# Optimization experiments

Hardware: AMD Instinct MI355X
Metric: run time of the kernel (lower is better)

The kernel has to match this reference:

```python
import jax, jax.numpy as jnp
import numpy as np

EMBED = 768
NH = 12          # num_heads
NL = 3           # num_levels
NP = 4           # num_points
DV = 384         # value dim = embed_dim * deform_ratio(0.5)
DH = DV // NH    # per-head value dim = 32
B = 16
LQ = 1024        # (512/16)^2 ViT tokens
SHAPES = [(64, 64), (32, 32), (16, 16)]  # 1/8, 1/16, 1/32 pyramid of 512x512
LKV = sum(h * w for h, w in SHAPES)      # 5376
EPS = 1e-6


def layer_norm(x, w, b):
    mu = jnp.mean(x, axis=-1, keepdims=True)
    var = jnp.mean((x - mu) ** 2, axis=-1, keepdims=True)
    return (x - mu) / jnp.sqrt(var + EPS) * w + b


def bilinear_sample(v, loc, H, W):
    # v: (B, NH, H*W, DH); loc: (B, Lq, NH, P, 2) normalized in [0,1]
    # Matches torch grid_sample(align_corners=False, padding_mode='zeros').
    Bv, Lq = loc.shape[0], loc.shape[1]
    x = loc[..., 0] * W - 0.5
    y = loc[..., 1] * H - 0.5
    x0 = jnp.floor(x)
    y0 = jnp.floor(y)
    dx = x - x0
    dy = y - y0
    x0i = x0.astype(jnp.int32)
    y0i = y0.astype(jnp.int32)

    def gather(xi, yi):
        valid = (xi >= 0) & (xi < W) & (yi >= 0) & (yi < H)  # (B,Lq,NH,P)
        xc = jnp.clip(xi, 0, W - 1)
        yc = jnp.clip(yi, 0, H - 1)
        lin = (yc * W + xc).transpose(0, 2, 1, 3).reshape(Bv, NH, Lq * NP)
        g = jnp.take_along_axis(v, lin[..., None], axis=2)  # (B,NH,Lq*P,DH)
        g = g.reshape(Bv, NH, Lq, NP, DH).transpose(0, 2, 1, 3, 4)  # (B,Lq,NH,P,DH)
        return g * valid[..., None].astype(g.dtype)

    g00 = gather(x0i, y0i)
    g01 = gather(x0i + 1, y0i)
    g10 = gather(x0i, y0i + 1)
    g11 = gather(x0i + 1, y0i + 1)
    w00 = ((1 - dx) * (1 - dy))[..., None]
    w01 = (dx * (1 - dy))[..., None]
    w10 = ((1 - dx) * dy)[..., None]
    w11 = (dx * dy)[..., None]
    return g00 * w00 + g01 * w01 + g10 * w10 + g11 * w11


def ms_deform_attn_core(value, shapes_list, loc, aw):
    # value: (B,LKV,NH,DH); loc: (B,Lq,NH,NL,NP,2); aw: (B,Lq,NH,NL,NP)
    Bv, Lq = loc.shape[0], loc.shape[1]
    samples = []
    idx = 0
    for l, (H, W) in enumerate(shapes_list):
        v = value[:, idx:idx + H * W].transpose(0, 2, 1, 3)  # (B,NH,HW,DH)
        idx += H * W
        samples.append(bilinear_sample(v, loc[:, :, :, l], H, W))
    s = jnp.stack(samples, axis=3)  # (B,Lq,NH,NL,NP,DH)
    o = jnp.einsum('bqhlp,bqhlpd->bqhd', aw, s)
    return o.reshape(Bv, Lq, NH * DH)


def setup_inputs() -> dict:
    key = jax.random.key(0)
    ks = jax.random.split(key, 12)

    def n(k, shape, s=0.02):
        return jax.random.normal(k, shape, jnp.float32) * s

    return {
        'q': jax.random.normal(ks[0], (B, LQ, EMBED), jnp.float32),
        'reference_points': jax.random.uniform(ks[1], (B, LQ, NL, 2), jnp.float32),
        'kv': jax.random.normal(ks[2], (B, LKV, EMBED), jnp.float32),
        'spatial_shapes': jnp.asarray(SHAPES, jnp.int32),
        'level_start_index': jnp.asarray(
            np.cumsum([0] + [h * w for h, w in SHAPES])[:-1], jnp.int32),
        'ln1_w': jnp.ones(EMBED, jnp.float32),
        'ln1_b': jnp.zeros(EMBED, jnp.float32),
        'ln2_w': jnp.ones(EMBED, jnp.float32),
        'ln2_b': jnp.zeros(EMBED, jnp.float32),
        'gamma': n(ks[3], (EMBED,), 0.1),
        'w_off': n(ks[4], (EMBED, NH * NL * NP * 2)),
        'b_off': n(ks[5], (NH * NL * NP * 2,), 0.01),
        'w_aw': n(ks[6], (EMBED, NH * NL * NP)),
        'b_aw': jnp.zeros(NH * NL * NP, jnp.float32),
        'w_val': n(ks[7], (EMBED, DV)),
        'b_val': jnp.zeros(DV, jnp.float32),
        'w_out': n(ks[8], (DV, EMBED)),
        'b_out': jnp.zeros(EMBED, jnp.float32),
    }


def reference(q, reference_points, kv, spatial_shapes, level_start_index,
              ln1_w, ln1_b, ln2_w, ln2_b, gamma,
              w_off, b_off, w_aw, b_aw, w_val, b_val, w_out, b_out):
    shapes_list = [tuple(int(v) for v in r) for r in np.asarray(spatial_shapes)]
    Bq, Lq, _ = q.shape
    qn = layer_norm(q, ln1_w, ln1_b)
    kvn = layer_norm(kv, ln2_w, ln2_b)
    value = (kvn @ w_val + b_val).reshape(Bq, -1, NH, DH)
    off = (qn @ w_off + b_off).reshape(Bq, Lq, NH, NL, NP, 2)
    aw = (qn @ w_aw + b_aw).reshape(Bq, Lq, NH, NL * NP)
    aw = jax.nn.softmax(aw, axis=-1).reshape(Bq, Lq, NH, NL, NP)
    # offset normalizer is (W_l, H_l) per level
    wh = jnp.asarray([[w, h] for (h, w) in shapes_list], q.dtype)  # (NL,2)
    loc = reference_points[:, :, None, :, None, :] + off / wh[None, None, None, :, None, :]
    attn = ms_deform_attn_core(value, shapes_list, loc, aw)
    attn = attn @ w_out + b_out
    return q + gamma * attn
```

## Files before the change

### kernel.cpp

```cpp
#include <hip/hip_runtime.h>

#define DEV __device__ __forceinline__

typedef short bf16x8 __attribute__((ext_vector_type(8)));
typedef short short8 __attribute__((ext_vector_type(8)));
typedef float f32x4 __attribute__((ext_vector_type(4)));
typedef unsigned int u32;
typedef __attribute__((address_space(1))) const u32* gas_ptr;
typedef __attribute__((address_space(3))) u32* las_ptr;

DEV short f2bf(float f) {
  union { float f; unsigned u; } un; un.f = f;
  unsigned r = un.u + 0x7FFFu + ((un.u >> 16) & 1u);
  return (short)(r >> 16);
}
DEV float bf2f(unsigned short s) {
  union { unsigned u; float f; } un;
  un.u = ((unsigned)s) << 16;
  return un.f;
}
DEV void gload16(const short* g, short* l) {
  __builtin_amdgcn_global_load_lds((gas_ptr)g, (las_ptr)l, 16, 0, 0);
}
DEV float hsum4(float4 v) { return v.x + v.y + v.z + v.w; }

DEV void ln_row4(const float* __restrict__ x, const float* __restrict__ w,
                 const float* __restrict__ b, short* __restrict__ y,
                 const int rb) {
  const int wv = threadIdx.x >> 6, lane = threadIdx.x & 63;
  const int row = rb * 4 + wv;
  const float* xr = x + (size_t)row * 768;
  float4 v0 = *(const float4*)(xr + lane * 4);
  float4 v1 = *(const float4*)(xr + 256 + lane * 4);
  float4 v2 = *(const float4*)(xr + 512 + lane * 4);
  float s = hsum4(v0) + hsum4(v1) + hsum4(v2);
  #pragma unroll
  for (int off = 32; off > 0; off >>= 1) s += __shfl_xor(s, off, 64);
  const float mu = s * (1.f / 768.f);
  float4 d0 = make_float4(v0.x - mu, v0.y - mu, v0.z - mu, v0.w - mu);
  float4 d1 = make_float4(v1.x - mu, v1.y - mu, v1.z - mu, v1.w - mu);
  float4 d2 = make_float4(v2.x - mu, v2.y - mu, v2.z - mu, v2.w - mu);
  float vs = d0.x * d0.x + d0.y * d0.y + d0.z * d0.z + d0.w * d0.w +
             d1.x * d1.x + d1.y * d1.y + d1.z * d1.z + d1.w * d1.w +
             d2.x * d2.x + d2.y * d2.y + d2.z * d2.z + d2.w * d2.w;
  #pragma unroll
  for (int off = 32; off > 0; off >>= 1) vs += __shfl_xor(vs, off, 64);
  const float rs = rsqrtf(vs * (1.f / 768.f) + 1e-6f);
  const float4 w0 = *(const float4*)(w + lane * 4);
  const float4 w1 = *(const float4*)(w + 256 + lane * 4);
  const float4 w2 = *(const float4*)(w + 512 + lane * 4);
  const float4 b0 = *(const float4*)(b + lane * 4);
  const float4 b1 = *(const float4*)(b + 256 + lane * 4);
  const float4 b2 = *(const float4*)(b + 512 + lane * 4);
  unsigned short* yr = (unsigned short*)y + (size_t)row * 768;
  ushort4 o;
  o.x = (unsigned short)f2bf(d0.x * rs * w0.x + b0.x);
  o.y = (unsigned short)f2bf(d0.y * rs * w0.y + b0.y);
  o.z = (unsigned short)f2bf(d0.z * rs * w0.z + b0.z);
  o.w = (unsigned short)f2bf(d0.w * rs * w0.w + b0.w);
  *(ushort4*)(yr + lane * 4) = o;
  o.x = (unsigned short)f2bf(d1.x * rs * w1.x + b1.x);
  o.y = (unsigned short)f2bf(d1.y * rs * w1.y + b1.y);
  o.z = (unsigned short)f2bf(d1.z * rs * w1.z + b1.z);
  o.w = (unsigned short)f2bf(d1.w * rs * w1.w + b1.w);
  *(ushort4*)(yr + 256 + lane * 4) = o;
  o.x = (unsigned short)f2bf(d2.x * rs * w2.x + b2.x);
  o.y = (unsigned short)f2bf(d2.y * rs * w2.y + b2.y);
  o.z = (unsigned short)f2bf(d2.z * rs * w2.z + b2.z);
  o.w = (unsigned short)f2bf(d2.w * rs * w2.w + b2.w);
  *(ushort4*)(yr + 512 + lane * 4) = o;
}

__global__ __launch_bounds__(256) void fused_pre_kernel(
    const float* __restrict__ kv, const float* __restrict__ q,
    const float* __restrict__ ln2w, const float* __restrict__ ln2b,
    const float* __restrict__ ln1w, const float* __restrict__ ln1b,
    short* __restrict__ kvn, short* __restrict__ qn,
    const float* __restrict__ w_val, const float* __restrict__ w_off,
    const float* __restrict__ w_aw, const float* __restrict__ w_out,
    const float* __restrict__ b_off, const float* __restrict__ b_aw,
    short* __restrict__ wT_val, short* __restrict__ wT_offaw,
    short* __restrict__ wT_out, float* __restrict__ bias_cat) {
  const int bid = blockIdx.x;
  if (bid < 21504) { ln_row4(kv, ln2w, ln2b, kvn, bid); return; }
  if (bid < 25600) { ln_row4(q, ln1w, ln1b, qn, bid - 21504); return; }
  int g = (bid - 25600) * 256 + threadIdx.x;
  bf16x8 v;
  if (g < 36864) {
    int n = g / 96, k0 = (g % 96) * 8;
    #pragma unroll
    for (int i = 0; i < 8; i++) v[i] = f2bf(w_val[(size_t)(k0 + i) * 384 + n]);
    *(bf16x8*)&wT_val[n * 768 + k0] = v;
    return;
  }
  g -= 36864;
  if (g < 27648) {
    int n = g / 96, k0 = (g % 96) * 8;
    #pragma unroll
    for (int i = 0; i < 8; i++) v[i] = f2bf(w_off[(size_t)(k0 + i) * 288 + n]);
    *(bf16x8*)&wT_offaw[n * 768 + k0] = v;
    return;
  }
  g -= 27648;
  if (g < 13824) {
    int n = g / 96, k0 = (g % 96) * 8;
    #pragma unroll
    for (int i = 0; i < 8; i++) v[i] = f2bf(w_aw[(size_t)(k0 + i) * 144 + n]);
    *(bf16x8*)&wT_offaw[(288 + n) * 768 + k0] = v;
    return;
  }
  g -= 13824;
  if (g < 7680) {
    int n = 432 + g / 96, k0 = (g % 96) * 8;
    #pragma unroll
    for (int i = 0; i < 8; i++) v[i] = 0;
    *(bf16x8*)&wT_offaw[n * 768 + k0] = v;
    return;
  }
  g -= 7680;
  if (g < 36864) {
    int n = g / 48, k0 = (g % 48) * 8;
    #pragma unroll
    for (int i = 0; i < 8; i++) v[i] = f2bf(w_out[(size_t)(k0 + i) * 768 + n]);
    *(bf16x8*)&wT_out[n * 384 + k0] = v;
    return;
  }
  g -= 36864;
  if (g < 512) { bias_cat[g] = (g < 288) ? b_off[g] : (g < 432 ? b_aw[g - 288] : 0.f); }
}

DEV void gemm_core(const short* __restrict__ A, const short* __restrict__ Wt,
                   const int K, const int row0, const int n0,
                   short* As, short* Bs, f32x4 acc[4][4]) {
  const int tid = threadIdx.x;
  const int wave = tid >> 6, lane = tid & 63;
  const int lr = lane & 15, quad = lane >> 4;
  const int wm = wave >> 1, wn = wave & 1;

  const short* gA[2]; const short* gB[2];
  int loA[2];
  #pragma unroll
  for (int rnd = 0; rnd < 2; rnd++) {
    int G = rnd * 256 + wave * 64 + lane;
    int line = G >> 3, pos = G & 7, x = pos ^ (line & 7);
    int r = line * 2 + (x >> 2), qk = (x & 3) * 8;
    gA[rnd] = A + (size_t)(row0 + r) * K + qk;
    gB[rnd] = Wt + (size_t)(n0 + r) * K + qk;
    loA[rnd] = (rnd * 256 + wave * 64) * 8;
  }

  int aOff[4], bOff[4];
  #pragma unroll
  for (int t4 = 0; t4 < 4; t4++) {
    int r = wm * 64 + t4 * 16 + lr;
    int pos = ((r & 1) * 4 + quad) ^ ((r >> 1) & 7);
    aOff[t4] = ((r >> 1) * 8 + pos) * 8;
    int rb = wn * 64 + t4 * 16 + lr;
    int posb = ((rb & 1) * 4 + quad) ^ ((rb >> 1) & 7);
    bOff[t4] = ((rb >> 1) * 8 + posb) * 8;
  }

  #pragma unroll
  for (int i = 0; i < 4; i++)
    #pragma unroll
    for (int j = 0; j < 4; j++)
      #pragma unroll
      for (int e = 0; e < 4; e++) acc[i][j][e] = 0.f;

  const int nt = K >> 5;
  #pragma unroll
  for (int pb = 0; pb < 2; pb++) {
    const int bb = pb * 4096;
    gload16(gA[0], As + bb + loA[0]);
    gload16(gA[1], As + bb + loA[1]);
    gload16(gB[0], Bs + bb + loA[0]);
    gload16(gB[1], Bs + bb + loA[1]);
    gA[0] += 32; gA[1] += 32; gB[0] += 32; gB[1] += 32;
  }

  int cur = 0;
  for (int t = 0; t < nt; ++t) {
    if (t + 2 < nt) {
      const int nb = (cur == 0 ? 2 : cur - 1) * 4096;
      gload16(gA[0], As + nb + loA[0]);
      gload16(gA[1], As + nb + loA[1]);
      gload16(gB[0], Bs + nb + loA[0]);
      gload16(gB[1], Bs + nb + loA[1]);
      gA[0] += 32; gA[1] += 32; gB[0] += 32; gB[1] += 32;
      asm volatile("s_waitcnt vmcnt(8)" ::: "memory");
    } else if (t + 1 < nt) {
      asm volatile("s_waitcnt vmcnt(4)" ::: "memory");
    } else {
      asm volatile("s_waitcnt vmcnt(0)" ::: "memory");
    }
    asm volatile("s_barrier" ::: "memory");
    const int cb = cur * 4096;
    bf16x8 av[4], bv[4];
    #pragma unroll
    for (int t4 = 0; t4 < 4; t4++) {
      av[t4] = *(const bf16x8*)(As + cb + aOff[t4]);
      bv[t4] = *(const bf16x8*)(Bs + cb + bOff[t4]);
    }
    #pragma unroll
    for (int ct = 0; ct < 4; ct++)
      #pragma unroll
      for (int rt = 0; rt < 4; rt++)
        acc[rt][ct] = __builtin_amdgcn_mfma_f32_16x16x32_bf16(av[rt], bv[ct], acc[rt][ct], 0, 0, 0);
    asm volatile("s_waitcnt lgkmcnt(0)" ::: "memory");
    __builtin_amdgcn_sched_barrier(0);
    asm volatile("s_barrier" ::: "memory");
    cur = (cur == 2) ? 0 : cur + 1;
  }
}

template <bool RES>
DEV void epilogue_f32(float* lds, f32x4 acc[4][4], const float* __restrict__ bias,
                      const float* __restrict__ qres, const float* __restrict__ gamma,
                      float* __restrict__ Cout, const int N,
                      const int row0, const int n0) {
  const int tid = threadIdx.x, wave = tid >> 6, lane = tid & 63;
  const int lr = lane & 15, quad = lane >> 4;
  const int wm = wave >> 1, wn = wave & 1;
  const int ST = 132;
  #pragma unroll
  for (int ph = 0; ph < 2; ++ph) {
    __syncthreads();
    if (wm == ph) {
      #pragma unroll
      for (int ct = 0; ct < 4; ct++)
        #pragma unroll
        for (int rt = 0; rt < 4; rt++)
          #pragma unroll
          for (int i = 0; i < 4; i++)
            lds[(rt * 16 + quad * 4 + i) * ST + wn * 64 + ct * 16 + lr] = acc[rt][ct][i];
    }
    __syncthreads();
    #pragma unroll
    for (int it = 0; it < 8; ++it) {
      const int slot = it * 256 + tid;
      const int r = slot >> 5, c4 = slot & 31;
      const float4 v = *(float4*)&lds[r * ST + c4 * 4];
      const int m = row0 + ph * 64 + r, n = n0 + c4 * 4;
      const float4 bs = *(const float4*)&bias[n];
      float4 o;
      if (RES) {
        const float4 qv = *(const float4*)&qres[(size_t)m * N + n];
        const float4 gm = *(const float4*)&gamma[n];
        o.x = qv.x + gm.x * (v.x + bs.x);
        o.y = qv.y + gm.y * (v.y + bs.y);
        o.z = qv.z + gm.z * (v.z + bs.z);
        o.w = qv.w + gm.w * (v.w + bs.w);
      } else {
        o.x = v.x + bs.x; o.y = v.y + bs.y; o.z = v.z + bs.z; o.w = v.w + bs.w;
      }
      *(float4*)&Cout[(size_t)m * N + n] = o;
    }
  }
}

DEV void epilogue_bf16(unsigned short* lds, f32x4 acc[4][4],
                       const float* __restrict__ bias,
                       unsigned short* __restrict__ Cout, const int N,
                       const int row0, const int n0) {
  const int tid = threadIdx.x, wave = tid >> 6, lane = tid & 63;
  const int lr = lane & 15, quad = lane >> 4;
  const int wm = wave >> 1, wn = wave & 1;
  const int ST = 136;
  #pragma unroll
  for (int ph = 0; ph < 2; ++ph) {
    __syncthreads();
    if (wm == ph) {
      #pragma unroll
      for (int ct = 0; ct < 4; ct++) {
        const float bs = bias[n0 + wn * 64 + ct * 16 + lr];
        #pragma unroll
        for (int rt = 0; rt < 4; rt++)
          #pragma unroll
          for (int i = 0; i < 4; i++)
            lds[(rt * 16 + quad * 4 + i) * ST + wn * 64 + ct * 16 + lr] =
                (unsigned short)f2bf(acc[rt][ct][i] + bs);
      }
    }
    __syncthreads();
    #pragma unroll
    for (int it = 0; it < 4; ++it) {
      const int slot = it * 256 + tid;
      const int r = slot >> 4, c8 = slot & 15;
      const short8 v = *(short8*)&lds[r * ST + c8 * 8];
      const int m = row0 + ph * 64 + r;
      *(short8*)&Cout[(size_t)m * N + n0 + c8 * 8] = v;
    }
  }
}

__global__ __launch_bounds__(256, 3) void gemm_dual_kernel(
    const short* __restrict__ A0, const short* __restrict__ W0,
    const float* __restrict__ b0, short* __restrict__ C0,
    const short* __restrict__ A1, const short* __restrict__ W1,
    const float* __restrict__ b1, float* __restrict__ C1) {
  __shared__ __align__(16) char smem[49152];
  short* As = (short*)smem;
  short* Bs = (short*)(smem + 24576);
  const int id = blockIdx.x;
  const int swz = (id & 7) * 316 + (id >> 3);
  const bool isval = swz < 2016;
  const short* A; const short* Wt; const float* bias;
  int row0, n0;
  if (isval) {
    A = A0; Wt = W0; bias = b0;
    n0 = (swz % 3) * 128; row0 = (swz / 3) * 128;
  } else {
    const int o = swz - 2016;
    A = A1; Wt = W1; bias = b1;
    n0 = (o & 3) * 128; row0 = (o >> 2) * 128;
  }
  f32x4 acc[4][4];
  gemm_core(A, Wt, 768, row0, n0, As, Bs, acc);
  if (isval) {
    epilogue_bf16((unsigned short*)smem, acc, bias, (unsigned short*)C0, 384, row0, n0);
  } else {
    epilogue_f32<false>((float*)smem, acc, bias, nullptr, nullptr, C1, 512, row0, n0);
  }
}

__global__ __launch_bounds__(256, 3) void gemm_final_kernel(
    const short* __restrict__ A, const short* __restrict__ Wt,
    const float* __restrict__ bias, const float* __restrict__ qres,
    const float* __restrict__ gamma, float* __restrict__ Cout) {
  __shared__ __align__(16) char smem[49152];
  short* As = (short*)smem;
  short* Bs = (short*)(smem + 24576);
  const int id = blockIdx.x;
  const int swz = (id & 7) * 96 + (id >> 3);
  const int n0 = (swz % 6) * 128, row0 = (swz / 6) * 128;
  f32x4 acc[4][4];
  gemm_core(A, Wt, 384, row0, n0, As, Bs, acc);
  epilogue_f32<true>((float*)smem, acc, bias, qres, gamma, Cout, 768, row0, n0);
}

__global__ __launch_bounds__(384) void sampler_kernel(
    const float* __restrict__ offaw,
    const float* __restrict__ refp,
    const short* __restrict__ value,
    short* __restrict__ o) {
  const int tid = threadIdx.x;
  const int blk = (blockIdx.x & 7) * 512 + (blockIdx.x >> 3);
  const int bq0 = blk * 4;
  __shared__ __align__(16) float s[4][440];
  __shared__ float sref[4][6];
  __shared__ float snw[48][12];
  __shared__ __align__(8) ushort4 slin[576];
  __shared__ __align__(16) float4 sw[576];

  {
    const int qi = tid / 96, t = tid % 96;
    const float* row = offaw + (size_t)(bq0 + qi) * 512;
    #pragma unroll
    for (int i = t; i < 108; i += 96)
      *(float4*)&s[qi][i * 4] = *(const float4*)&row[i * 4];
    if (t < 6) sref[qi][t] = refp[(size_t)(bq0 + qi) * 6 + t];
  }
  __syncthreads();

  if (tid < 48) {
    const int qi = tid / 12, h = tid % 12;
    const float* awp = &s[qi][288 + h * 12];
    float mx = awp[0];
    #pragma unroll
    for (int j = 1; j < 12; j++) mx = fmaxf(mx, awp[j]);
    float e[12], ssum = 0.f;
    #pragma unroll
    for (int j = 0; j < 12; j++) { e[j] = __expf(awp[j] - mx); ssum += e[j]; }
    const float inv = 1.f / ssum;
    #pragma unroll
    for (int j = 0; j < 12; j++) snw[tid][j] = e[j] * inv;
  }
  for (int tu = tid; tu < 576; tu += 384) {
    const int qi = tu / 144, rem = tu % 144;
    const int h = rem / 12, lp = rem % 12, l = lp >> 2, p = lp & 3;
    const int Wi = 64 >> l;
    const float Wf = (float)Wi;
    const float rx = sref[qi][l * 2], ry = sref[qi][l * 2 + 1];
    const int oi = ((h * 3 + l) * 4 + p) * 2;
    float x = fmaf(rx, Wf, s[qi][oi] - 0.5f);
    float y = fmaf(ry, Wf, s[qi][oi + 1] - 0.5f);
    float xf = floorf(x), yf = floorf(y);
    float dx = x - xf, dy = y - yf;
    int x0 = (int)xf, y0 = (int)yf;
    int x1 = x0 + 1, y1 = y0 + 1;
    int x0c = min(max(x0, 0), Wi - 1), x1c = min(max(x1, 0), Wi - 1);
    int y0c = min(max(y0, 0), Wi - 1), y1c = min(max(y1, 0), Wi - 1);
    float wx0 = (x0 >= 0 && x0 < Wi) ? (1.f - dx) : 0.f;
    float wx1 = (x1 < Wi && x1 >= 0) ? dx : 0.f;
    float wy0 = (y0 >= 0 && y0 < Wi) ? (1.f - dy) : 0.f;
    float wy1 = (y1 < Wi && y1 >= 0) ? dy : 0.f;
    const int st = (l == 0) ? 0 : (l == 1 ? 4096 : 5120);
    ushort4 lv;
    lv.x = (unsigned short)(st + y0c * Wi + x0c);
    lv.y = (unsigned short)(st + y0c * Wi + x1c);
    lv.z = (unsigned short)(st + y1c * Wi + x0c);
    lv.w = (unsigned short)(st + y1c * Wi + x1c);
    slin[tu] = lv;
    sw[tu] = make_float4(wx0 * wy0, wx1 * wy0, wx0 * wy1, wx1 * wy1);
  }
  __syncthreads();

  const int qi = tid / 96, t = tid % 96;
  const int head = t >> 3, ln4 = t & 7;
  const int bq = bq0 + qi;
  const int b = bq >> 10;
  const unsigned short* vb =
      (const unsigned short*)value + (size_t)b * 5376 * 384 + head * 32 + ln4 * 4;
  float4 acc = make_float4(0.f, 0.f, 0.f, 0.f);
  const int tub = qi * 144 + head * 12;
  const float* nwp = snw[qi * 12 + head];
  #pragma unroll
  for (int lp = 0; lp < 12; lp++) {
    const int tu = tub + lp;
    const float g = nwp[lp];
    const ushort4 lv = slin[tu];
    const float4 wv = sw[tu];
    const ushort4 u00 = *(const ushort4*)(vb + (size_t)lv.x * 384);
    const ushort4 u01 = *(const ushort4*)(vb + (size_t)lv.y * 384);
    const ushort4 u10 = *(const ushort4*)(vb + (size_t)lv.z * 384);
    const ushort4 u11 = *(const ushort4*)(vb + (size_t)lv.w * 384);
    const float w00 = g * wv.x, w01 = g * wv.y, w10 = g * wv.z, w11 = g * wv.w;
    acc.x += w00 * bf2f(u00.x) + w01 * bf2f(u01.x) + w10 * bf2f(u10.x) + w11 * bf2f(u11.x);
    acc.y += w00 * bf2f(u00.y) + w01 * bf2f(u01.y) + w10 * bf2f(u10.y) + w11 * bf2f(u11.y);
    acc.z += w00 * bf2f(u00.z) + w01 * bf2f(u01.z) + w10 * bf2f(u10.z) + w11 * bf2f(u11.z);
    acc.w += w00 * bf2f(u00.w) + w01 * bf2f(u01.w) + w10 * bf2f(u10.w) + w11 * bf2f(u11.w);
  }
  ushort4 outv;
  outv.x = (unsigned short)f2bf(acc.x);
  outv.y = (unsigned short)f2bf(acc.y);
  outv.z = (unsigned short)f2bf(acc.z);
  outv.w = (unsigned short)f2bf(acc.w);
  *(ushort4*)((unsigned short*)o + (size_t)bq * 384 + head * 32 + ln4 * 4) = outv;
}

extern "C" void kernel_launch(void* const* d_in, const int* in_sizes, int n_in,
                              void* d_out, int out_size, void* d_ws, size_t ws_size,
                              hipStream_t stream) {
  (void)in_sizes; (void)n_in; (void)out_size; (void)ws_size;
  const float* q     = (const float*)d_in[0];
  const float* refp  = (const float*)d_in[1];
  const float* kv    = (const float*)d_in[2];
  const float* ln1w  = (const float*)d_in[5];
  const float* ln1b  = (const float*)d_in[6];
  const float* ln2w  = (const float*)d_in[7];
  const float* ln2b  = (const float*)d_in[8];
  const float* gamma = (const float*)d_in[9];
  const float* w_off = (const float*)d_in[10];
  const float* b_off = (const float*)d_in[11];
  const float* w_aw  = (const float*)d_in[12];
  const float* b_aw  = (const float*)d_in[13];
  const float* w_val = (const float*)d_in[14];
  const float* b_val = (const float*)d_in[15];
  const float* w_out = (const float*)d_in[16];
  const float* b_out = (const float*)d_in[17];
  float* out = (float*)d_out;

  char* wsp = (char*)d_ws;
  size_t cur = 0;
  auto alloc = [&](size_t bytes) -> void* {
    cur = (cur + 255) & ~(size_t)255;
    void* p = wsp + cur;
    cur += bytes;
    return p;
  };
  short*  wT_val   = (short*)alloc((size_t)384 * 768 * 2);
  short*  wT_offaw = (short*)alloc((size_t)512 * 768 * 2);
  short*  wT_out   = (short*)alloc((size_t)768 * 384 * 2);
  float*  bias_cat = (float*)alloc((size_t)512 * 4);
  short*  kvn      = (short*)alloc((size_t)86016 * 768 * 2);
  short*  qn       = (short*)alloc((size_t)16384 * 768 * 2);
  short*  value    = (short*)alloc((size_t)86016 * 384 * 2);
  float*  offaw    = (float*)alloc((size_t)16384 * 512 * 4);
  short*  obuf     = (short*)alloc((size_t)16384 * 384 * 2);

  fused_pre_kernel<<<26082, 256, 0, stream>>>(
      kv, q, ln2w, ln2b, ln1w, ln1b, kvn, qn,
      w_val, w_off, w_aw, w_out, b_off, b_aw,
      wT_val, wT_offaw, wT_out, bias_cat);
  gemm_dual_kernel<<<2528, 256, 0, stream>>>(
      kvn, wT_val, b_val, value, qn, wT_offaw, bias_cat, offaw);
  sampler_kernel<<<4096, 384, 0, stream>>>(offaw, refp, value, obuf);
  gemm_final_kernel<<<768, 256, 0, stream>>>(
      obuf, wT_out, b_out, q, gamma, out);
}
```

Measured before the change: 615.6 us.

## Use 256x128 tiles with 512-thread blocks for the dual value/offset GEMM

The dual GEMM moves from 128x128 tiles on 256 threads to 256x128 tiles on 512 threads (8 waves). A new core loads twice the A rows per stage into a larger triple-buffered LDS region, so each B tile is reused across more rows. The epilogues are widened to cover four 64-row phases. This halves the block count and cuts B-operand traffic, at the cost of 72KB LDS per block, which lowers the number of resident blocks per CU.

```diff
diff --git a/kernel.cpp b/kernel.cpp
--- a/kernel.cpp
+++ b/kernel.cpp
@@ -213,6 +213,94 @@
   }
 }
 
+DEV void gemm_core256(const short* __restrict__ A, const short* __restrict__ Wt,
+                      const int K, const int row0, const int n0,
+                      short* As, short* Bs, f32x4 acc[4][4]) {
+  const int tid = threadIdx.x;
+  const int wave = tid >> 6, lane = tid & 63;
+  const int lr = lane & 15, quad = lane >> 4;
+  const int wm = wave >> 1, wn = wave & 1;
+
+  const short* gA[2]; const short* gB;
+  int loA[2], loB;
+  #pragma unroll
+  for (int rnd = 0; rnd < 2; rnd++) {
+    int G = rnd * 512 + tid;
+    int line = G >> 3, pos = G & 7, x = pos ^ (line & 7);
+    int r = line * 2 + (x >> 2), qk = (x & 3) * 8;
+    gA[rnd] = A + (size_t)(row0 + r) * K + qk;
+    loA[rnd] = G * 8;
+  }
+  {
+    int G = tid;
+    int line = G >> 3, pos = G & 7, x = pos ^ (line & 7);
+    int r = line * 2 + (x >> 2), qk = (x & 3) * 8;
+    gB = Wt + (size_t)(n0 + r) * K + qk;
+    loB = G * 8;
+  }
+
+  int aOff[4], bOff[4];
+  #pragma unroll
+  for (int t4 = 0; t4 < 4; t4++) {
+    int r = wm * 64 + t4 * 16 + lr;
+    int pos = ((r & 1) * 4 + quad) ^ ((r >> 1) & 7);
+    aOff[t4] = ((r >> 1) * 8 + pos) * 8;
+    int rb = wn * 64 + t4 * 16 + lr;
+    int posb = ((rb & 1) * 4 + quad) ^ ((rb >> 1) & 7);
+    bOff[t4] = ((rb >> 1) * 8 + posb) * 8;
+  }
+
+  #pragma unroll
+  for (int i = 0; i < 4; i++)
+    #pragma unroll
+    for (int j = 0; j < 4; j++)
+      #pragma unroll
+      for (int e = 0; e < 4; e++) acc[i][j][e] = 0.f;
+
+  const int nt = K >> 5;
+  #pragma unroll
+  for (int pb = 0; pb < 2; pb++) {
+    gload16(gA[0], As + pb * 8192 + loA[0]);
+    gload16(gA[1], As + pb * 8192 + loA[1]);
+    gload16(gB,    Bs + pb * 4096 + loB);
+    gA[0] += 32; gA[1] += 32; gB += 32;
+  }
+
+  int cur = 0;
+  for (int t = 0; t < nt; ++t) {
+    if (t + 2 < nt) {
+      const int nb = (cur == 0 ? 2 : cur - 1);
+      gload16(gA[0], As + nb * 8192 + loA[0]);
+      gload16(gA[1], As + nb * 8192 + loA[1]);
+      gload16(gB,    Bs + nb * 4096 + loB);
+      gA[0] += 32; gA[1] += 32; gB += 32;
+      asm volatile("s_waitcnt vmcnt(6)" ::: "memory");
+    } else if (t + 1 < nt) {
+      asm volatile("s_waitcnt vmcnt(3)" ::: "memory");
+    } else {
+      asm volatile("s_waitcnt vmcnt(0)" ::: "memory");
+    }
+    asm volatile("s_barrier" ::: "memory");
+    const short* Ab = As + cur * 8192;
+    const short* Bb = Bs + cur * 4096;
+    bf16x8 av[4], bv[4];
+    #pragma unroll
+    for (int t4 = 0; t4 < 4; t4++) {
+      av[t4] = *(const bf16x8*)(Ab + aOff[t4]);
+      bv[t4] = *(const bf16x8*)(Bb + bOff[t4]);
+    }
+    #pragma unroll
+    for (int ct = 0; ct < 4; ct++)
+      #pragma unroll
+      for (int rt = 0; rt < 4; rt++)
+        acc[rt][ct] = __builtin_amdgcn_mfma_f32_16x16x32_bf16(av[rt], bv[ct], acc[rt][ct], 0, 0, 0);
+    asm volatile("s_waitcnt lgkmcnt(0)" ::: "memory");
+    __builtin_amdgcn_sched_barrier(0);
+    asm volatile("s_barrier" ::: "memory");
+    cur = (cur == 2) ? 0 : cur + 1;
+  }
+}
+
 template <bool RES>
 DEV void epilogue_f32(float* lds, f32x4 acc[4][4], const float* __restrict__ bias,
                       const float* __restrict__ qres, const float* __restrict__ gamma,
@@ -258,16 +346,50 @@
   }
 }
 
-DEV void epilogue_bf16(unsigned short* lds, f32x4 acc[4][4],
-                       const float* __restrict__ bias,
-                       unsigned short* __restrict__ Cout, const int N,
-                       const int row0, const int n0) {
+DEV void epilogue256_f32(float* lds, f32x4 acc[4][4], const float* __restrict__ bias,
+                         float* __restrict__ Cout, const int N,
+                         const int row0, const int n0) {
+  const int tid = threadIdx.x, wave = tid >> 6, lane = tid & 63;
+  const int lr = lane & 15, quad = lane >> 4;
+  const int wm = wave >> 1, wn = wave & 1;
+  const int ST = 132;
+  #pragma unroll
+  for (int ph = 0; ph < 4; ++ph) {
+    __syncthreads();
+    if (wm == ph) {
+      #pragma unroll
+      for (int ct = 0; ct < 4; ct++)
+        #pragma unroll
+        for (int rt = 0; rt < 4; rt++)
+          #pragma unroll
+          for (int i = 0; i < 4; i++)
+            lds[(rt * 16 + quad * 4 + i) * ST + wn * 64 + ct * 16 + lr] = acc[rt][ct][i];
+    }
+    __syncthreads();
+    #pragma unroll
+    for (int it = 0; it < 4; ++it) {
+      const int slot = it * 512 + tid;
+      const int r = slot >> 5, c4 = slot & 31;
+      const float4 v = *(float4*)&lds[r * ST + c4 * 4];
+      const int m = row0 + ph * 64 + r, n = n0 + c4 * 4;
+      const float4 bs = *(const float4*)&bias[n];
+      float4 o;
+      o.x = v.x + bs.x; o.y = v.y + bs.y; o.z = v.z + bs.z; o.w = v.w + bs.w;
+      *(float4*)&Cout[(size_t)m * N + n] = o;
+    }
+  }
+}
+
+DEV void epilogue256_bf16(unsigned short* lds, f32x4 acc[4][4],
+                          const float* __restrict__ bias,
+                          unsigned short* __restrict__ Cout, const int N,
+                          const int row0, const int n0) {
   const int tid = threadIdx.x, wave = tid >> 6, lane = tid & 63;
   const int lr = lane & 15, quad = lane >> 4;
   const int wm = wave >> 1, wn = wave & 1;
   const int ST = 136;
   #pragma unroll
-  for (int ph = 0; ph < 2; ++ph) {
+  for (int ph = 0; ph < 4; ++ph) {
     __syncthreads();
     if (wm == ph) {
       #pragma unroll
@@ -283,8 +405,8 @@
     }
     __syncthreads();
     #pragma unroll
-    for (int it = 0; it < 4; ++it) {
-      const int slot = it * 256 + tid;
+    for (int it = 0; it < 2; ++it) {
+      const int slot = it * 512 + tid;
       const int r = slot >> 4, c8 = slot & 15;
       const short8 v = *(short8*)&lds[r * ST + c8 * 8];
       const int m = row0 + ph * 64 + r;
@@ -293,33 +415,33 @@
   }
 }
 
-__global__ __launch_bounds__(256, 3) void gemm_dual_kernel(
+__global__ __launch_bounds__(512, 4) void gemm_dual_kernel(
     const short* __restrict__ A0, const short* __restrict__ W0,
     const float* __restrict__ b0, short* __restrict__ C0,
     const short* __restrict__ A1, const short* __restrict__ W1,
     const float* __restrict__ b1, float* __restrict__ C1) {
-  __shared__ __align__(16) char smem[49152];
+  __shared__ __align__(16) char smem[73728];
   short* As = (short*)smem;
-  short* Bs = (short*)(smem + 24576);
+  short* Bs = (short*)(smem + 49152);
   const int id = blockIdx.x;
-  const int swz = (id & 7) * 316 + (id >> 3);
-  const bool isval = swz < 2016;
+  const int swz = (id & 7) * 158 + (id >> 3);
+  const bool isval = swz < 1008;
   const short* A; const short* Wt; const float* bias;
   int row0, n0;
   if (isval) {
     A = A0; Wt = W0; bias = b0;
-    n0 = (swz % 3) * 128; row0 = (swz / 3) * 128;
+    n0 = (swz % 3) * 128; row0 = (swz / 3) * 256;
   } else {
-    const int o = swz - 2016;
+    const int o = swz - 1008;
     A = A1; Wt = W1; bias = b1;
-    n0 = (o & 3) * 128; row0 = (o >> 2) * 128;
+    n0 = (o & 3) * 128; row0 = (o >> 2) * 256;
   }
   f32x4 acc[4][4];
-  gemm_core(A, Wt, 768, row0, n0, As, Bs, acc);
+  gemm_core256(A, Wt, 768, row0, n0, As, Bs, acc);
   if (isval) {
-    epilogue_bf16((unsigned short*)smem, acc, bias, (unsigned short*)C0, 384, row0, n0);
+    epilogue256_bf16((unsigned short*)smem, acc, bias, (unsigned short*)C0, 384, row0, n0);
   } else {
-    epilogue_f32<false>((float*)smem, acc, bias, nullptr, nullptr, C1, 512, row0, n0);
+    epilogue256_f32((float*)smem, acc, bias, C1, 512, row0, n0);
   }
 }
 
@@ -482,7 +604,7 @@
       kv, q, ln2w, ln2b, ln1w, ln1b, kvn, qn,
       w_val, w_off, w_aw, w_out, b_off, b_aw,
       wT_val, wT_offaw, wT_out, bias_cat);
-  gemm_dual_kernel<<<2528, 256, 0, stream>>>(
+  gemm_dual_kernel<<<1264, 512, 0, stream>>>(
       kvn, wT_val, b_val, value, qn, wT_offaw, bias_cat, offaw);
   sampler_kernel<<<4096, 384, 0, stream>>>(offaw, refp, value, obuf);
   gemm_final_kernel<<<768, 256, 0, stream>>>(
```

After: 621.4 us. No clear change (+1.0%).
